# Performance work log

Measured on AMD Instinct MI355X. Metric: run time of the kernel, lower is better.

## Reference

```python
import jax, jax.numpy as jnp
import numpy as np

B, C, H, W = 4096, 1, 64, 64
NCLASS = 10
ALPHA = 1.0
EPS = 1e-8  # torch CosineSimilarity eps


def setup_inputs() -> dict:
    key = jax.random.key(0)
    k1, k2, k3 = jax.random.split(key, 3)
    outputs = jax.random.normal(k1, (B, NCLASS), dtype=jnp.float32)
    grad = jax.random.normal(k2, (B, C, H, W), dtype=jnp.float32)
    y = jax.random.randint(k3, (B,), 0, NCLASS)
    return {"outputs": outputs, "grad": grad, "y": y}


def reference(outputs, grad, y):
    b = grad.shape[0]
    # per-sample min-max normalization over all of (C,H,W)
    flat = grad.reshape(b, -1)                      # [B, C*H*W]
    gmax = flat.max(axis=1, keepdims=True)
    gmin = flat.min(axis=1, keepdims=True)
    ngrad = (flat - gmin) / (gmax - gmin)           # [B, D]

    # batched pairwise cosine similarity: normalize + matmul
    norms = jnp.linalg.norm(ngrad, axis=1, keepdims=True)
    vn = ngrad / jnp.maximum(norms, EPS)
    sim = vn @ vn.T                                 # [B, B]

    # pairs (i<j) with the same predicted class (argmax(softmax(o)) == argmax(o))
    pred = jnp.argmax(outputs, axis=1)
    same = pred[:, None] == pred[None, :]
    upper = jnp.triu(jnp.ones((b, b), dtype=bool), k=1)
    mask = same & upper
    xloss = jnp.sum(jnp.where(mask, 1.0 - sim, 0.0)) / b

    # cross-entropy
    logp = jax.nn.log_softmax(outputs, axis=1)
    celoss = -jnp.take_along_axis(logp, y[:, None], axis=1).sum() / b
    return celoss + ALPHA * xloss
```

## Files before the change

kernel.cpp:

```cpp
#include <hip/hip_runtime.h>
#include <math.h>

constexpr int Dn = 4096;
constexpr int Bn = 4096;
constexpr int NCLS = 10;
constexpr int CH = 4;
constexpr int NBLK0 = Bn / 256;
constexpr int MAXCH = Bn / CH + NCLS;

constexpr int OFF_CEB  = 0;
constexpr int OFF_CNT  = 16;
constexpr int OFF_XS   = 176;
constexpr int OFF_DONE = 177;
constexpr int OFF_ORDB = 192;
constexpr int OFF_P    = 41216;

__global__ __launch_bounds__(256) void pass0_ce_order(
    const float* __restrict__ outputs, const int* __restrict__ y,
    float* __restrict__ ws)
{
    const int t = threadIdx.x;
    const int b = blockIdx.x;
    const int i = b * 256 + t;
    const int w = t >> 6, lane = t & 63;
    int* wsi = (int*)ws;

    __shared__ int hist[NCLS];
    __shared__ float sce[4];
    if (t < NCLS) hist[t] = 0;
    __syncthreads();

    const float* o = outputs + (size_t)i * NCLS;
    float m = o[0]; int am = 0;
    #pragma unroll
    for (int k = 1; k < NCLS; ++k) { float ok = o[k]; if (ok > m) { m = ok; am = k; } }
    float se = 0.f;
    #pragma unroll
    for (int k = 0; k < NCLS; ++k) se += expf(o[k] - m);
    float ce = m + logf(se) - o[y[i]];

    int rank = atomicAdd(&hist[am], 1);
    wsi[OFF_ORDB + (b * NCLS + am) * 256 + rank] = i;

    #pragma unroll
    for (int off = 32; off; off >>= 1) ce += __shfl_down(ce, off, 64);
    if (lane == 0) sce[w] = ce;
    __syncthreads();

    if (t < NCLS) wsi[OFF_CNT + b * NCLS + t] = hist[t];
    if (t == 0) ws[OFF_CEB + b] = sce[0] + sce[1] + sce[2] + sce[3];
    if (b == 0 && t == 32) { ws[OFF_XS] = 0.f; wsi[OFF_DONE] = 0; }
}

__global__ __launch_bounds__(256) void pass12_fused(
    const float* __restrict__ grad, float* __restrict__ ws)
{
    const int* wsi = (const int*)ws;
    const int t = threadIdx.x, w = t >> 6, lane = t & 63;

    __shared__ int lcnt[NBLK0 * NCLS];
    __shared__ int tot[NCLS];
    if (t < NBLK0 * NCLS) lcnt[t] = wsi[OFF_CNT + t];
    __syncthreads();
    if (t < NCLS) {
        int s = 0;
        #pragma unroll
        for (int bb = 0; bb < NBLK0; ++bb) s += lcnt[bb * NCLS + t];
        tot[t] = s;
    }
    __syncthreads();

    int c = -1, s0 = 0, cnt = 0;
    {
        int bidx = (int)blockIdx.x, acc = 0;
        #pragma unroll
        for (int k = 0; k < NCLS; ++k) {
            int n = tot[k];
            int nch = (n + CH - 1) / CH;
            if (c < 0 && bidx < acc + nch) { c = k; s0 = (bidx - acc) * CH; cnt = n; }
            acc += nch;
        }
    }
    if (c < 0) return;
    const int m = min(CH, cnt - s0);

    float4 v[16];
    if (w < m) {
        int idx;
        {
            const int r = s0 + w;
            int pref = 0, src = 0, loc = 0;
            #pragma unroll
            for (int bb = 0; bb < NBLK0; ++bb) {
                int n = lcnt[bb * NCLS + c];
                if (r >= pref && r < pref + n) { src = bb; loc = r - pref; }
                pref += n;
            }
            idx = wsi[OFF_ORDB + (src * NCLS + c) * 256 + loc];
        }
        const float4* row = (const float4*)grad + (size_t)idx * (Dn / 4);
        #pragma unroll
        for (int k = 0; k < 16; ++k) v[k] = row[k * 64 + lane];

        float mn = fminf(fminf(v[0].x, v[0].y), fminf(v[0].z, v[0].w));
        #pragma unroll
        for (int k = 1; k < 16; ++k)
            mn = fminf(mn, fminf(fminf(v[k].x, v[k].y), fminf(v[k].z, v[k].w)));
        #pragma unroll
        for (int off = 1; off < 64; off <<= 1)
            mn = fminf(mn, __shfl_xor(mn, off, 64));

        float ss = 0.f;
        #pragma unroll
        for (int k = 0; k < 16; ++k) {
            float dx = v[k].x - mn, dy = v[k].y - mn;
            float dz = v[k].z - mn, dw = v[k].w - mn;
            ss += dx * dx + dy * dy + dz * dz + dw * dw;
        }
        #pragma unroll
        for (int off = 1; off < 64; off <<= 1)
            ss += __shfl_xor(ss, off, 64);

        const float a = 1.0f / sqrtf(ss);
        const float b = -mn * a;
        #pragma unroll
        for (int k = 0; k < 16; ++k) {
            v[k].x = fmaf(v[k].x, a, b);
            v[k].y = fmaf(v[k].y, a, b);
            v[k].z = fmaf(v[k].z, a, b);
            v[k].w = fmaf(v[k].w, a, b);
        }
    } else {
        #pragma unroll
        for (int k = 0; k < 16; ++k) v[k] = make_float4(0.f, 0.f, 0.f, 0.f);
    }

    __shared__ float4 buf[1024];
    if (w == 1) {
        #pragma unroll
        for (int k = 0; k < 16; ++k) buf[k * 64 + lane] = v[k];
    }
    __syncthreads();
    if (w == 0) {
        #pragma unroll
        for (int k = 0; k < 16; ++k) {
            float4 u = buf[k * 64 + lane];
            v[k].x += u.x; v[k].y += u.y; v[k].z += u.z; v[k].w += u.w;
        }
    }
    __syncthreads();
    if (w == 3) {
        #pragma unroll
        for (int k = 0; k < 16; ++k) buf[k * 64 + lane] = v[k];
    }
    __syncthreads();
    if (w == 2) {
        #pragma unroll
        for (int k = 0; k < 16; ++k) {
            float4 u = buf[k * 64 + lane];
            v[k].x += u.x; v[k].y += u.y; v[k].z += u.z; v[k].w += u.w;
            buf[k * 64 + lane] = v[k];
        }
    }
    __syncthreads();
    if (w == 0) {
        float4* Pc = (float4*)(ws + OFF_P) + (size_t)blockIdx.x * (Dn / 4);
        #pragma unroll
        for (int k = 0; k < 16; ++k) {
            float4 u = buf[k * 64 + lane];
            v[k].x += u.x; v[k].y += u.y; v[k].z += u.z; v[k].w += u.w;
            Pc[k * 64 + lane] = v[k];
        }
    }
}

__global__ __launch_bounds__(256) void pass34_final(
    float* __restrict__ ws, float* __restrict__ out)
{
    const int t = threadIdx.x;
    const int idx = blockIdx.x * 256 + t;
    const int c = idx >> 12;
    const int j = idx & (Dn - 1);
    const int w = t >> 6, lane = t & 63;
    const int* wsi = (const int*)ws;

    __shared__ int tot[NCLS];
    if (t < NCLS) {
        int s = 0;
        #pragma unroll
        for (int bb = 0; bb < NBLK0; ++bb) s += wsi[OFF_CNT + bb * NCLS + t];
        tot[t] = s;
    }
    __syncthreads();

    int cs = 0, ce2 = 0;
    {
        int acc = 0;
        #pragma unroll
        for (int k = 0; k < NCLS; ++k) {
            int nch = (tot[k] + CH - 1) / CH;
            if (k == c) { cs = acc; ce2 = acc + nch; }
            acc += nch;
        }
    }

    const float* P = ws + OFF_P;
    float s = 0.f;
    int ch = cs;
    for (; ch + 4 <= ce2; ch += 4)
        s += P[(size_t)(ch + 0) * Dn + j] + P[(size_t)(ch + 1) * Dn + j]
           + P[(size_t)(ch + 2) * Dn + j] + P[(size_t)(ch + 3) * Dn + j];
    for (; ch < ce2; ++ch) s += P[(size_t)ch * Dn + j];
    float p = s * s;

    #pragma unroll
    for (int off = 32; off; off >>= 1) p += __shfl_down(p, off, 64);
    __shared__ float sr[4];
    if (lane == 0) sr[w] = p;
    __syncthreads();
    if (t == 0) {
        atomicAdd(&ws[OFF_XS], sr[0] + sr[1] + sr[2] + sr[3]);
        __threadfence();
        int ticket = atomicAdd(&((int*)ws)[OFF_DONE], 1);
        if (ticket == (NCLS * Dn / 256) - 1) {
            float xs = atomicAdd(&ws[OFF_XS], 0.0f);
            double n2 = 0.0;
            #pragma unroll
            for (int k = 0; k < NCLS; ++k) { double nc = (double)tot[k]; n2 += nc * nc; }
            double cesum = 0.0;
            #pragma unroll
            for (int k = 0; k < NBLK0; ++k) cesum += (double)ws[OFF_CEB + k];
            double xloss = (n2 - (double)xs) / (2.0 * (double)Bn);
            out[0] = (float)(cesum / (double)Bn + xloss);
        }
    }
}

extern "C" void kernel_launch(void* const* d_in, const int* in_sizes, int n_in,
                              void* d_out, int out_size, void* d_ws, size_t ws_size,
                              hipStream_t stream)
{
    const float* outputs = (const float*)d_in[0];
    const float* grad    = (const float*)d_in[1];
    const int*   y       = (const int*)d_in[2];
    float* ws  = (float*)d_ws;
    float* out = (float*)d_out;

    pass0_ce_order<<<NBLK0, 256, 0, stream>>>(outputs, y, ws);
    pass12_fused<<<MAXCH, 256, 0, stream>>>(grad, ws);
    pass34_final<<<NCLS * Dn / 256, 256, 0, stream>>>(ws, out);
}
```

Measured before the change: 116.9 us.

## Sum 16 rows per block via swizzled LDS atomics in 1024-thread blocks

The fused normalize-and-sum kernel now handles 16 rows per block with 1024 threads instead of 4 rows with 256 threads. The staged shared-memory tree reduction is replaced by float atomicAdd into an LDS accumulator, with a swizzle across the four float components to spread bank conflicts, followed by an unswizzle at write-out. This writes 4x fewer partial vectors and lets the final pass read 4x fewer chunks per class, at the cost of LDS atomic contention from 16 waves and fewer, larger blocks.

```diff
diff --git a/kernel.cpp b/kernel.cpp
--- a/kernel.cpp
+++ b/kernel.cpp
@@ -4,7 +4,7 @@
 constexpr int Dn = 4096;
 constexpr int Bn = 4096;
 constexpr int NCLS = 10;
-constexpr int CH = 4;
+constexpr int CH = 16;
 constexpr int NBLK0 = Bn / 256;
 constexpr int MAXCH = Bn / CH + NCLS;
 
@@ -52,7 +52,7 @@
     if (b == 0 && t == 32) { ws[OFF_XS] = 0.f; wsi[OFF_DONE] = 0; }
 }
 
-__global__ __launch_bounds__(256) void pass12_fused(
+__global__ __launch_bounds__(1024) void pass12_fused(
     const float* __restrict__ grad, float* __restrict__ ws)
 {
     const int* wsi = (const int*)ws;
@@ -60,13 +60,16 @@
 
     __shared__ int lcnt[NBLK0 * NCLS];
     __shared__ int tot[NCLS];
+    __shared__ float lbuf[Dn];
+
+    ((float4*)lbuf)[t] = make_float4(0.f, 0.f, 0.f, 0.f);
     if (t < NBLK0 * NCLS) lcnt[t] = wsi[OFF_CNT + t];
     __syncthreads();
     if (t < NCLS) {
-        int s = 0;
-        #pragma unroll
-        for (int bb = 0; bb < NBLK0; ++bb) s += lcnt[bb * NCLS + t];
-        tot[t] = s;
+        int sum = 0;
+        #pragma unroll
+        for (int bb = 0; bb < NBLK0; ++bb) sum += lcnt[bb * NCLS + t];
+        tot[t] = sum;
     }
     __syncthreads();
 
@@ -83,8 +86,8 @@
     }
     if (c < 0) return;
     const int m = min(CH, cnt - s0);
-
-    float4 v[16];
+    const int s = (lane >> 3) & 3;
+
     if (w < m) {
         int idx;
         {
@@ -99,6 +102,7 @@
             idx = wsi[OFF_ORDB + (src * NCLS + c) * 256 + loc];
         }
         const float4* row = (const float4*)grad + (size_t)idx * (Dn / 4);
+        float4 v[16];
         #pragma unroll
         for (int k = 0; k < 16; ++k) v[k] = row[k * 64 + lane];
 
@@ -123,54 +127,26 @@
 
         const float a = 1.0f / sqrtf(ss);
         const float b = -mn * a;
+
         #pragma unroll
         for (int k = 0; k < 16; ++k) {
-            v[k].x = fmaf(v[k].x, a, b);
-            v[k].y = fmaf(v[k].y, a, b);
-            v[k].z = fmaf(v[k].z, a, b);
-            v[k].w = fmaf(v[k].w, a, b);
-        }
-    } else {
-        #pragma unroll
-        for (int k = 0; k < 16; ++k) v[k] = make_float4(0.f, 0.f, 0.f, 0.f);
-    }
-
-    __shared__ float4 buf[1024];
-    if (w == 1) {
-        #pragma unroll
-        for (int k = 0; k < 16; ++k) buf[k * 64 + lane] = v[k];
-    }
-    __syncthreads();
-    if (w == 0) {
-        #pragma unroll
-        for (int k = 0; k < 16; ++k) {
-            float4 u = buf[k * 64 + lane];
-            v[k].x += u.x; v[k].y += u.y; v[k].z += u.z; v[k].w += u.w;
-        }
-    }
-    __syncthreads();
-    if (w == 3) {
-        #pragma unroll
-        for (int k = 0; k < 16; ++k) buf[k * 64 + lane] = v[k];
-    }
-    __syncthreads();
-    if (w == 2) {
-        #pragma unroll
-        for (int k = 0; k < 16; ++k) {
-            float4 u = buf[k * 64 + lane];
-            v[k].x += u.x; v[k].y += u.y; v[k].z += u.z; v[k].w += u.w;
-            buf[k * 64 + lane] = v[k];
-        }
-    }
-    __syncthreads();
-    if (w == 0) {
+            const int bk = k * 256 + 4 * lane;
+            atomicAdd(&lbuf[bk + (s ^ 0)], fmaf(v[k].x, a, b));
+            atomicAdd(&lbuf[bk + (s ^ 1)], fmaf(v[k].y, a, b));
+            atomicAdd(&lbuf[bk + (s ^ 2)], fmaf(v[k].z, a, b));
+            atomicAdd(&lbuf[bk + (s ^ 3)], fmaf(v[k].w, a, b));
+        }
+    }
+    __syncthreads();
+
+    {
+        float4 u = ((const float4*)lbuf)[t];
+        const int st = (t >> 3) & 3;
+        float a0 = u.x, a1 = u.y, a2 = u.z, a3 = u.w;
+        if (st & 1) { float tm = a0; a0 = a1; a1 = tm; tm = a2; a2 = a3; a3 = tm; }
+        if (st & 2) { float tm = a0; a0 = a2; a2 = tm; tm = a1; a1 = a3; a3 = tm; }
         float4* Pc = (float4*)(ws + OFF_P) + (size_t)blockIdx.x * (Dn / 4);
-        #pragma unroll
-        for (int k = 0; k < 16; ++k) {
-            float4 u = buf[k * 64 + lane];
-            v[k].x += u.x; v[k].y += u.y; v[k].z += u.z; v[k].w += u.w;
-            Pc[k * 64 + lane] = v[k];
-        }
+        Pc[t] = make_float4(a0, a1, a2, a3);
     }
 }
 
@@ -247,6 +223,6 @@
     float* out = (float*)d_out;
 
     pass0_ce_order<<<NBLK0, 256, 0, stream>>>(outputs, y, ws);
-    pass12_fused<<<MAXCH, 256, 0, stream>>>(grad, ws);
+    pass12_fused<<<MAXCH, 1024, 0, stream>>>(grad, ws);
     pass34_final<<<NCLS * Dn / 256, 256, 0, stream>>>(ws, out);
 }
```

Measured after the change: 267.1 us. 128% more time.
